# Optimization experiments

Hardware: AMD Instinct MI355X
Metric: run time of the kernel (lower is better)

Reference implementation:

```python
import jax, jax.numpy as jnp
import numpy as np

TARGET_FRAMES = 16
VOXEL_LAMBDA = 20.0
CONF_THRESHOLD = 0.1
CONF_PERCENTILE = 50.0
G = 48  # per-axis voxel grid cap (lambda=20 => ~20-40 occupied cells/axis for randn points)


def setup_inputs() -> dict:
    key = jax.random.key(0)
    k1, k2, k3, k4, k5 = jax.random.split(key, 5)
    B, S, H, W = 1, 128, 224, 224
    return {
        "depth": jax.random.uniform(k1, (B, S, H, W, 1), dtype=jnp.float32),
        "depth_conf": jax.random.uniform(k2, (B, S, H, W), dtype=jnp.float32),
        "world_points": jax.random.normal(k3, (B, S, H, W, 3), dtype=jnp.float32),
        "world_points_conf": jax.random.uniform(k4, (B, S, H, W), dtype=jnp.float32),
        "pose_enc": jax.random.normal(k5, (B, S, 9), dtype=jnp.float32),
    }


def _voxel_occupancy(world_points, world_points_conf):
    # world_points: [1,S,H,W,3], conf: [1,S,H,W]
    pts = world_points[0].reshape(world_points.shape[1], -1, 3)   # [S, HW, 3]
    conf = world_points_conf[0].reshape(world_points.shape[1], -1)  # [S, HW]
    # per-frame confidence filter: conf > thr AND conf >= per-frame percentile
    pct = jnp.quantile(conf, CONF_PERCENTILE / 100.0, axis=1)       # [S]
    valid = (conf > CONF_THRESHOLD) & (conf >= pct[:, None])        # [S, HW]
    big = jnp.float32(1e30)
    pmin = jnp.min(jnp.where(valid[..., None], pts, big), axis=(0, 1))   # [3]
    pmax = jnp.max(jnp.where(valid[..., None], pts, -big), axis=(0, 1))  # [3]
    voxel_size = jnp.min(pmax - pmin) / VOXEL_LAMBDA  # adaptive voxel size
    idx = jnp.floor((pts - pmin) / voxel_size).astype(jnp.int32)
    idx = jnp.clip(idx, 0, G - 1)
    vid = (idx[..., 0] * G + idx[..., 1]) * G + idx[..., 2]  # [S, HW]
    V = G * G * G
    vid = jnp.where(valid, vid, V)  # invalid points -> trash bin V
    S = pts.shape[0]
    occ = jnp.zeros((S, V + 1), dtype=bool).at[jnp.arange(S)[:, None], vid].set(True)
    return occ[:, :V]  # [S, V] per-frame voxel occupancy bitmaps


def _greedy_max_coverage(occ, k):
    S, V = occ.shape

    def step(carry, _):
        covered, selected = carry  # [V] bool, [S] bool
        gains = jnp.sum(occ & ~covered[None, :], axis=1).astype(jnp.float32)  # [S]
        gains = jnp.where(selected, -1.0, gains)
        best = jnp.argmax(gains)  # first max == greedy in-order tie-break
        covered = covered | occ[best]
        selected = selected.at[best].set(True)
        return (covered, selected), (best.astype(jnp.int32), gains[best])

    (covered, _), (sel, scores) = jax.lax.scan(
        step, (jnp.zeros((V,), bool), jnp.zeros((S,), bool)), None, length=k)
    return sel, scores, covered


def reference(depth, depth_conf, world_points, world_points_conf, pose_enc):
    occ = _voxel_occupancy(world_points, world_points_conf)
    sel, scores, covered = _greedy_max_coverage(occ, TARGET_FRAMES)
    total_coverage = jnp.sum(covered).astype(jnp.int32)
    # selected_indices [1,K], coverage_scores [1,K], total_coverage scalar
    return sel[None, :], scores[None, :], total_coverage
```

## Files before the change

kernel.cpp:

```cpp
#include <hip/hip_runtime.h>
#include <hip/hip_bf16.h>
#include <cstdint>

#define S_FRAMES 128
#define HW       50176
#define NGRP     12544
#define GDIM     48
#define VWORDS   3456
#define NBINS    4096
#define CAP      512
#define KSEL     16

#define GBLK     16
#define FPB      8
#define GW       4

#define OCCA_OFF  0u
#define OCCB_OFF  (128u*3456u)
#define SLOT_OFF  (2u*128u*3456u)
#define MM_OFF    (SLOT_OFF + 512u)
#define PCT_OFF   (MM_OFF + 64u*16u)
#define ZERO_OFF  SLOT_OFF
#define ZERO_WORDS (PCT_OFF - SLOT_OFF)

__device__ __forceinline__ unsigned fkey(float f) {
    unsigned u = __float_as_uint(f);
    return (u & 0x80000000u) ? ~u : (u | 0x80000000u);
}
__device__ __forceinline__ float funkey(unsigned k) {
    unsigned u = (k & 0x80000000u) ? (k & 0x7fffffffu) : ~k;
    return __uint_as_float(u);
}

__global__ __launch_bounds__(1024) void pct_kernel(const float* __restrict__ conf,
                                                   float* __restrict__ pct) {
    const int s = blockIdx.x;
    const int tid = threadIdx.x;
    const int lane = tid & 63, wid = tid >> 6;
    const float4* c4 = (const float4*)(conf + (size_t)s * HW);

    __shared__ unsigned hist[NBINS];
    __shared__ unsigned wtot[16];
    __shared__ unsigned woff[16];
    __shared__ float    list[CAP];
    __shared__ unsigned cnt;
    __shared__ int      rbin[2];
    __shared__ unsigned rcum[2];
    __shared__ float    ab[2];

    for (int b = tid; b < NBINS; b += 1024) hist[b] = 0;
    if (tid == 0) cnt = 0;
    __syncthreads();

    for (int g = tid; g < NGRP; g += 1024) {
        float4 v = c4[g];
        int b0 = min(max((int)(v.x * 4096.0f), 0), NBINS - 1);
        int b1 = min(max((int)(v.y * 4096.0f), 0), NBINS - 1);
        int b2 = min(max((int)(v.z * 4096.0f), 0), NBINS - 1);
        int b3 = min(max((int)(v.w * 4096.0f), 0), NBINS - 1);
        atomicAdd(&hist[b0], 1u); atomicAdd(&hist[b1], 1u);
        atomicAdd(&hist[b2], 1u); atomicAdd(&hist[b3], 1u);
    }
    __syncthreads();

    unsigned chunk = hist[tid * 4] + hist[tid * 4 + 1] + hist[tid * 4 + 2] + hist[tid * 4 + 3];
    unsigned x = chunk;
#pragma unroll
    for (int m = 1; m < 64; m <<= 1) {
        unsigned y = (unsigned)__shfl_up((int)x, m);
        if (lane >= m) x += y;
    }
    if (lane == 63) wtot[wid] = x;
    __syncthreads();
    if (tid < 16) {
        unsigned acc = 0;
        for (int w = 0; w < tid; w++) acc += wtot[w];
        woff[tid] = acc;
    }
    __syncthreads();
    unsigned excl = x - chunk + woff[wid];

    const unsigned R0 = 25087u, R1 = 25088u;
#pragma unroll
    for (int r = 0; r < 2; r++) {
        unsigned rr = r ? R1 : R0;
        if (rr >= excl && rr < excl + chunk) {
            unsigned cum = excl;
            for (int j = 0; j < 4; j++) {
                unsigned h = hist[tid * 4 + j];
                if (rr < cum + h) { rbin[r] = tid * 4 + j; rcum[r] = cum; break; }
                cum += h;
            }
        }
    }
    __syncthreads();

    const int blo = rbin[0], bhi = rbin[1];
    const unsigned cumLo = rcum[0];

    for (int g = tid; g < NGRP; g += 1024) {
        float4 v = c4[g];
        float vv[4] = {v.x, v.y, v.z, v.w};
#pragma unroll
        for (int j = 0; j < 4; j++) {
            int b = min(max((int)(vv[j] * 4096.0f), 0), NBINS - 1);
            if (b >= blo && b <= bhi) {
                unsigned pos = atomicAdd(&cnt, 1u);
                if (pos < CAP) list[pos] = vv[j];
            }
        }
    }
    __syncthreads();

    const int n = (int)min(cnt, (unsigned)CAP);
    const int r0 = (int)(R0 - cumLo), r1 = (int)(R1 - cumLo);
    for (int e = tid; e < n; e += 1024) {
        float xx = list[e];
        int rank = 0;
        for (int j = 0; j < n; j++) {
            float y = list[j];
            rank += (y < xx) || (y == xx && j < e);
        }
        if (rank == r0) ab[0] = xx;
        if (rank == r1) ab[1] = xx;
    }
    __syncthreads();
    if (tid == 0) pct[s] = 0.5f * ab[0] + 0.5f * ab[1];
}

__global__ __launch_bounds__(256) void minmax_kernel(const float* __restrict__ wp,
                                                     const float* __restrict__ conf,
                                                     const float* __restrict__ pct,
                                                     unsigned* __restrict__ ws) {
    const int s = blockIdx.y;
    const int tid = threadIdx.x;
    const int gidx = blockIdx.x * 256 + tid;
    const float pc = pct[s];
    const size_t base = (size_t)s * HW;

    const float4 cf = ((const float4*)(conf + base))[gidx];
    const float4* wp4 = (const float4*)(wp + base * 3) + (size_t)gidx * 3;
    const float4 a = wp4[0], b = wp4[1], d = wp4[2];

    const float BIG = 3.402823466e38f;
    float mnx = BIG, mny = BIG, mnz = BIG;
    float mxx = -BIG, mxy = -BIG, mxz = -BIG;

    float px[4] = {a.x, a.w, b.z, d.y};
    float py[4] = {a.y, b.x, b.w, d.z};
    float pz[4] = {a.z, b.y, d.x, d.w};
    float cc[4] = {cf.x, cf.y, cf.z, cf.w};
#pragma unroll
    for (int j = 0; j < 4; j++) {
        bool v = (cc[j] > 0.1f) && (cc[j] >= pc);
        float x = v ? px[j] : BIG, y = v ? py[j] : BIG, z = v ? pz[j] : BIG;
        mnx = fminf(mnx, x); mny = fminf(mny, y); mnz = fminf(mnz, z);
        x = v ? px[j] : -BIG; y = v ? py[j] : -BIG; z = v ? pz[j] : -BIG;
        mxx = fmaxf(mxx, x); mxy = fmaxf(mxy, y); mxz = fmaxf(mxz, z);
    }
#pragma unroll
    for (int m = 32; m >= 1; m >>= 1) {
        mnx = fminf(mnx, __shfl_xor(mnx, m)); mny = fminf(mny, __shfl_xor(mny, m));
        mnz = fminf(mnz, __shfl_xor(mnz, m));
        mxx = fmaxf(mxx, __shfl_xor(mxx, m)); mxy = fmaxf(mxy, __shfl_xor(mxy, m));
        mxz = fmaxf(mxz, __shfl_xor(mxz, m));
    }
    __shared__ float red[4][6];
    if ((tid & 63) == 0) {
        int w = tid >> 6;
        red[w][0] = mnx; red[w][1] = mny; red[w][2] = mnz;
        red[w][3] = mxx; red[w][4] = mxy; red[w][5] = mxz;
    }
    __syncthreads();
    if (tid == 0) {
        float r0 = red[0][0], r1 = red[0][1], r2 = red[0][2];
        float r3 = red[0][3], r4 = red[0][4], r5 = red[0][5];
        for (int w = 1; w < 4; w++) {
            r0 = fminf(r0, red[w][0]); r1 = fminf(r1, red[w][1]); r2 = fminf(r2, red[w][2]);
            r3 = fmaxf(r3, red[w][3]); r4 = fmaxf(r4, red[w][4]); r5 = fmaxf(r5, red[w][5]);
        }
        unsigned* slot = ws + MM_OFF + (unsigned)((blockIdx.x + blockIdx.y * 49) & 63) * 16;
        atomicMax(slot + 0, fkey(-r0));
        atomicMax(slot + 1, fkey(-r1));
        atomicMax(slot + 2, fkey(-r2));
        atomicMax(slot + 3, fkey(r3));
        atomicMax(slot + 4, fkey(r4));
        atomicMax(slot + 5, fkey(r5));
    }
}

__global__ __launch_bounds__(512) void voxel_kernel(const float* __restrict__ wp,
                                                    const float* __restrict__ conf,
                                                    const float* __restrict__ pct,
                                                    unsigned* __restrict__ ws) {
    const int s = blockIdx.x >> 1;
    const int part = blockIdx.x & 1;
    const int tid = threadIdx.x;

    __shared__ unsigned bm[VWORDS];
    __shared__ float prm[4];
    for (int w = tid; w < VWORDS; w += 512) bm[w] = 0;

    if (tid < 64) {
        const unsigned* sl = ws + MM_OFF + (unsigned)tid * 16;
        unsigned k0 = sl[0], k1 = sl[1], k2 = sl[2], k3 = sl[3], k4 = sl[4], k5 = sl[5];
#pragma unroll
        for (int m = 32; m >= 1; m >>= 1) {
            k0 = max(k0, (unsigned)__shfl_xor((int)k0, m));
            k1 = max(k1, (unsigned)__shfl_xor((int)k1, m));
            k2 = max(k2, (unsigned)__shfl_xor((int)k2, m));
            k3 = max(k3, (unsigned)__shfl_xor((int)k3, m));
            k4 = max(k4, (unsigned)__shfl_xor((int)k4, m));
            k5 = max(k5, (unsigned)__shfl_xor((int)k5, m));
        }
        if (tid == 0) {
            float p0 = -funkey(k0), p1 = -funkey(k1), p2 = -funkey(k2);
            float d0 = funkey(k3) - p0, d1 = funkey(k4) - p1, d2 = funkey(k5) - p2;
            prm[0] = p0; prm[1] = p1; prm[2] = p2;
            prm[3] = fminf(d0, fminf(d1, d2)) / 20.0f;
        }
    }
    __syncthreads();

    const float pc = pct[s];
    const float pmx = prm[0], pmy = prm[1], pmz = prm[2], vs = prm[3];
    const size_t base = (size_t)s * HW;
    const float4* c4 = (const float4*)(conf + base);
    const float4* w4 = (const float4*)(wp + base * 3);

#pragma unroll 1
    for (int k = 0; k < 13; k++) {
        int gl = k * 512 + tid;
        if (gl >= 6272) break;
        int g = part * 6272 + gl;
        float4 cf = c4[g];
        const float4* wg = w4 + (size_t)g * 3;
        float4 a = wg[0], b = wg[1], d = wg[2];
        float px[4] = {a.x, a.w, b.z, d.y};
        float py[4] = {a.y, b.x, b.w, d.z};
        float pz[4] = {a.z, b.y, d.x, d.w};
        float cc[4] = {cf.x, cf.y, cf.z, cf.w};
#pragma unroll
        for (int j = 0; j < 4; j++) {
            if (cc[j] > 0.1f && cc[j] >= pc) {
                int ix = min(max((int)floorf((px[j] - pmx) / vs), 0), GDIM - 1);
                int iy = min(max((int)floorf((py[j] - pmy) / vs), 0), GDIM - 1);
                int iz = min(max((int)floorf((pz[j] - pmz) / vs), 0), GDIM - 1);
                int vid = (ix * GDIM + iy) * GDIM + iz;
                atomicOr(&bm[vid >> 5], 1u << (vid & 31));
            }
        }
    }
    __syncthreads();

    unsigned* occ = ws + (part ? OCCB_OFF : OCCA_OFF) + (unsigned)s * VWORDS;
    for (int w = tid; w < VWORDS; w += 512) occ[w] = bm[w];
}

__global__ __launch_bounds__(1024) void greedy_kernel(unsigned* __restrict__ ws,
                                                      float* __restrict__ out) {
    const int b = blockIdx.x;
    const int tid = threadIdx.x;
    const int lane = tid & 63, wid = tid >> 6;
    const unsigned* pA = ws + OCCA_OFF;
    const unsigned* pB = ws + OCCB_OFF;
    unsigned* slots = ws + SLOT_OFF;

    unsigned occ[FPB][GW], cov[GW];
#pragma unroll
    for (int k = 0; k < GW; k++) cov[k] = 0u;
#pragma unroll
    for (int j = 0; j < FPB; j++) {
        unsigned f = (unsigned)(b * FPB + j);
#pragma unroll
        for (int k = 0; k < GW; k++) {
            int w = tid + k * 1024;
            occ[j][k] = (w < VWORDS) ? (pA[f * VWORDS + w] | pB[f * VWORDS + w]) : 0u;
        }
    }

    __shared__ int part[16][FPB];
    __shared__ unsigned bbc;
    unsigned selMask = 0;
    int best = -1;

    for (int it = 0; it < KSEL; it++) {
        if (best >= 0) {
            const unsigned* bA = pA + (unsigned)best * VWORDS;
            const unsigned* bB = pB + (unsigned)best * VWORDS;
#pragma unroll
            for (int k = 0; k < GW; k++) {
                int w = tid + k * 1024;
                if (w < VWORDS) cov[k] |= bA[w] | bB[w];
            }
        }
#pragma unroll
        for (int j = 0; j < FPB; j++) {
            int g = 0;
#pragma unroll
            for (int k = 0; k < GW; k++) g += __popc(occ[j][k] & ~cov[k]);
#pragma unroll
            for (int m = 32; m >= 1; m >>= 1) g += __shfl_xor(g, m);
            if (lane == 0) part[wid][j] = g;
        }
        __syncthreads();
        if (wid == 0) {
            unsigned key = 0;
            if (lane < FPB) {
                int g = 0;
#pragma unroll
                for (int w = 0; w < 16; w++) g += part[w][lane];
                int f = b * FPB + lane;
                key = ((selMask >> lane) & 1u) ? 0u
                    : (((unsigned)g << 7) | (unsigned)(127 - f));
            }
#pragma unroll
            for (int m = 4; m >= 1; m >>= 1) key = max(key, (unsigned)__shfl_xor((int)key, m));
            if (lane == 0)
                __hip_atomic_store(&slots[b * 32 + it], key | 0x80000000u,
                                   __ATOMIC_RELAXED, __HIP_MEMORY_SCOPE_AGENT);
            unsigned p = 0;
            if (lane < GBLK) {
                unsigned v;
                do {
                    v = __hip_atomic_load(&slots[lane * 32 + it],
                                          __ATOMIC_RELAXED, __HIP_MEMORY_SCOPE_AGENT);
                } while (!(v & 0x80000000u));
                p = v & 0x7fffffffu;
            }
#pragma unroll
            for (int m = 8; m >= 1; m >>= 1) p = max(p, (unsigned)__shfl_xor((int)p, m));
            if (lane == 0) bbc = p;
        }
        __syncthreads();
        unsigned kk = bbc;
        best = 127 - (int)(kk & 127u);
        if (best >= b * FPB && best < (b + 1) * FPB) selMask |= 1u << (best - b * FPB);
        if (b == 0 && tid == 0) {
            out[it] = (float)best;
            out[KSEL + it] = (float)(kk >> 7);
        }
        __syncthreads();
    }

    if (b == 0) {
        const unsigned* bA = pA + (unsigned)best * VWORDS;
        const unsigned* bB = pB + (unsigned)best * VWORDS;
        int t = 0;
#pragma unroll
        for (int k = 0; k < GW; k++) {
            int w = tid + k * 1024;
            if (w < VWORDS) t += __popc(cov[k] | bA[w] | bB[w]);
        }
#pragma unroll
        for (int m = 32; m >= 1; m >>= 1) t += __shfl_xor(t, m);
        if (lane == 0) part[wid][0] = t;
        __syncthreads();
        if (tid == 0) {
            int tt = 0;
            for (int w = 0; w < 16; w++) tt += part[w][0];
            out[2 * KSEL] = (float)tt;
        }
    }
}

extern "C" void kernel_launch(void* const* d_in, const int* in_sizes, int n_in,
                              void* d_out, int out_size, void* d_ws, size_t ws_size,
                              hipStream_t stream) {
    const float* wp   = (const float*)d_in[2];
    const float* conf = (const float*)d_in[3];
    float* out = (float*)d_out;
    unsigned* ws = (unsigned*)d_ws;

    hipMemsetAsync(ws + ZERO_OFF, 0, (size_t)ZERO_WORDS * 4, stream);

    float* pct = (float*)(ws + PCT_OFF);
    pct_kernel<<<128, 1024, 0, stream>>>(conf, pct);
    minmax_kernel<<<dim3(49, 128), 256, 0, stream>>>(wp, conf, pct, ws);
    voxel_kernel<<<256, 512, 0, stream>>>(wp, conf, pct, ws);
    greedy_kernel<<<GBLK, 1024, 0, stream>>>(ws, out);
}
```

Baseline: 261.1 us.

## Compact occupancy bitmaps to union-occupied voxels and run single-block greedy

Adds a union pass over all frame bitmaps, then remaps each frame's occupancy into a compact bitmap indexed by the rank of each voxel among occupied voxels. When the occupied count fits a cap, a single-block greedy kernel keeps each frame's compact bitmap in registers and does all sixteen selection steps inside one block with shared-memory coverage, avoiding cross-block coordination. The original multi-block greedy becomes a fallback gated by a workspace flag. This adds three kernel launches and extra bitmap passes in exchange for a much smaller greedy working set.

```diff
diff --git a/kernel.cpp b/kernel.cpp
--- a/kernel.cpp
+++ b/kernel.cpp
@@ -15,11 +15,19 @@
 #define FPB      8
 #define GW       4
 
+#define UWC      512u
+#define UCAP_BITS 16384u
+#define SLW      64
+
 #define OCCA_OFF  0u
 #define OCCB_OFF  (128u*3456u)
 #define SLOT_OFF  (2u*128u*3456u)
 #define MM_OFF    (SLOT_OFF + 512u)
 #define PCT_OFF   (MM_OFF + 64u*16u)
+#define FLAG_OFF  (PCT_OFF + 128u)
+#define UW_OFF    (FLAG_OFF + 1u)
+#define UNI_OFF   (FLAG_OFF + 16u)
+#define CMP_OFF   (UNI_OFF + VWORDS)
 #define ZERO_OFF  SLOT_OFF
 #define ZERO_WORDS (PCT_OFF - SLOT_OFF)
 
@@ -257,8 +265,161 @@
     for (int w = tid; w < VWORDS; w += 512) occ[w] = bm[w];
 }
 
+__global__ __launch_bounds__(256) void union_kernel(unsigned* __restrict__ ws) {
+    int w = blockIdx.x * 256 + threadIdx.x;
+    if (w >= VWORDS) return;
+    const unsigned* pA = ws + OCCA_OFF;
+    const unsigned* pB = ws + OCCB_OFF;
+    unsigned u = 0;
+#pragma unroll 4
+    for (int f = 0; f < S_FRAMES; f++)
+        u |= pA[(unsigned)f * VWORDS + w] | pB[(unsigned)f * VWORDS + w];
+    ws[UNI_OFF + w] = u;
+}
+
+__global__ __launch_bounds__(256) void remap_kernel(unsigned* __restrict__ ws) {
+    const int f = blockIdx.x;
+    const int tid = threadIdx.x;
+    const int lane = tid & 63, wid = tid >> 6;
+
+    __shared__ unsigned uni[VWORDS];
+    __shared__ unsigned short basew[VWORDS];
+    __shared__ unsigned cbm[UWC];
+    __shared__ unsigned wtot[4];
+    __shared__ unsigned Ush;
+
+    for (int w = tid; w < VWORDS; w += 256) uni[w] = ws[UNI_OFF + w];
+    for (int w = tid; w < (int)UWC; w += 256) cbm[w] = 0;
+    __syncthreads();
+
+    const int w0 = tid * 14;
+    unsigned chunk = 0;
+#pragma unroll
+    for (int j = 0; j < 14; j++) { int w = w0 + j; if (w < VWORDS) chunk += __popc(uni[w]); }
+    unsigned x = chunk;
+#pragma unroll
+    for (int m = 1; m < 64; m <<= 1) {
+        unsigned y = (unsigned)__shfl_up((int)x, m);
+        if (lane >= m) x += y;
+    }
+    if (lane == 63) wtot[wid] = x;
+    __syncthreads();
+    unsigned woffv = 0;
+    for (int wv = 0; wv < 4; wv++) if (wv < wid) woffv += wtot[wv];
+    unsigned running = x - chunk + woffv;
+#pragma unroll
+    for (int j = 0; j < 14; j++) {
+        int w = w0 + j;
+        if (w < VWORDS) { basew[w] = (unsigned short)running; running += __popc(uni[w]); }
+    }
+    if (tid == 255) Ush = running;
+    __syncthreads();
+    const unsigned U = Ush;
+    if (f == 0 && tid == 0) { ws[FLAG_OFF] = (U <= UCAP_BITS) ? 2u : 1u; ws[UW_OFF] = (U + 31) >> 5; }
+    if (U > UCAP_BITS) return;
+
+    const unsigned* pA = ws + OCCA_OFF + (unsigned)f * VWORDS;
+    const unsigned* pB = ws + OCCB_OFF + (unsigned)f * VWORDS;
+    for (int w = tid; w < VWORDS; w += 256) {
+        unsigned v = pA[w] | pB[w];
+        if (!v) continue;
+        unsigned uw = uni[w], b0 = basew[w];
+        while (v) {
+            int b = __ffs(v) - 1; v &= v - 1;
+            unsigned cid = b0 + (unsigned)__popc(uw & ((1u << b) - 1u));
+            atomicOr(&cbm[cid >> 5], 1u << (cid & 31));
+        }
+    }
+    __syncthreads();
+    const unsigned UW = (U + 31) >> 5;
+    for (unsigned w = tid; w < UW; w += 256) ws[CMP_OFF + (unsigned)f * UWC + w] = cbm[w];
+}
+
+__global__ __launch_bounds__(1024) void greedy1_kernel(unsigned* __restrict__ ws,
+                                                       float* __restrict__ out) {
+    if (ws[FLAG_OFF] != 2u) return;
+    const int tid = threadIdx.x;
+    const int f = tid >> 3, sl = tid & 7;
+    const unsigned UW = ws[UW_OFF];
+    const int sw = (int)((UW + 7) >> 3);
+    const int wbase = sl * sw;
+
+    __shared__ unsigned cov[UWC];
+    __shared__ int gains[S_FRAMES];
+    __shared__ unsigned bestsh;
+
+    unsigned occw[SLW];
+    const unsigned* cmp = ws + CMP_OFF + (unsigned)f * UWC;
+#pragma unroll
+    for (int j = 0; j < SLW; j++) {
+        int w = wbase + j;
+        occw[j] = (j < sw && w < (int)UW) ? cmp[w] : 0u;
+    }
+    for (int w = tid; w < (int)UWC; w += 1024) cov[w] = 0u;
+
+    bool selF = false;
+    int best = -1;
+    __syncthreads();
+
+    for (int it = 0; it < KSEL; it++) {
+        if (best >= 0 && f == best) {
+#pragma unroll
+            for (int j = 0; j < SLW; j++) {
+                int w = wbase + j;
+                if (j < sw && w < (int)UW) cov[w] |= occw[j];
+            }
+        }
+        __syncthreads();
+        int g = 0;
+#pragma unroll
+        for (int j = 0; j < SLW; j++) {
+            int w = wbase + j;
+            if (j < sw && w < (int)UW) g += __popc(occw[j] & ~cov[w]);
+        }
+        g += __shfl_xor(g, 1); g += __shfl_xor(g, 2); g += __shfl_xor(g, 4);
+        if (sl == 0) gains[f] = selF ? -1 : g;
+        __syncthreads();
+        if (tid < 64) {
+            int g1 = gains[tid], g2 = gains[tid + 64];
+            unsigned k1 = (g1 < 0) ? 0u : (((unsigned)g1 << 7) | (unsigned)(127 - tid));
+            unsigned k2 = (g2 < 0) ? 0u : (((unsigned)g2 << 7) | (unsigned)(63 - tid));
+            unsigned k = max(k1, k2);
+#pragma unroll
+            for (int m = 32; m >= 1; m >>= 1) k = max(k, (unsigned)__shfl_xor((int)k, m));
+            if (tid == 0) {
+                bestsh = k;
+                out[it] = (float)(127 - (int)(k & 127u));
+                out[KSEL + it] = (float)(k >> 7);
+            }
+        }
+        __syncthreads();
+        best = 127 - (int)(bestsh & 127u);
+        if (f == best) selF = true;
+    }
+
+    if (f == best) {
+#pragma unroll
+        for (int j = 0; j < SLW; j++) {
+            int w = wbase + j;
+            if (j < sw && w < (int)UW) cov[w] |= occw[j];
+        }
+    }
+    __syncthreads();
+    if (f == 0) {
+        int t = 0;
+#pragma unroll
+        for (int j = 0; j < SLW; j++) {
+            int w = wbase + j;
+            if (j < sw && w < (int)UW) t += __popc(cov[w]);
+        }
+        t += __shfl_xor(t, 1); t += __shfl_xor(t, 2); t += __shfl_xor(t, 4);
+        if (sl == 0) out[2 * KSEL] = (float)t;
+    }
+}
+
 __global__ __launch_bounds__(1024) void greedy_kernel(unsigned* __restrict__ ws,
                                                       float* __restrict__ out) {
+    if (ws[FLAG_OFF] == 2u) return;
     const int b = blockIdx.x;
     const int tid = threadIdx.x;
     const int lane = tid & 63, wid = tid >> 6;
@@ -378,5 +539,8 @@
     pct_kernel<<<128, 1024, 0, stream>>>(conf, pct);
     minmax_kernel<<<dim3(49, 128), 256, 0, stream>>>(wp, conf, pct, ws);
     voxel_kernel<<<256, 512, 0, stream>>>(wp, conf, pct, ws);
+    union_kernel<<<14, 256, 0, stream>>>(ws);
+    remap_kernel<<<128, 256, 0, stream>>>(ws);
+    greedy1_kernel<<<1, 1024, 0, stream>>>(ws, out);
     greedy_kernel<<<GBLK, 1024, 0, stream>>>(ws, out);
 }
```

Result: slower. 280.3 us (+7.4%).
